# Optimization experiments

Measured on AMD Instinct MI355X. Metric: run time of the kernel, lower is better.

The kernel has to match this reference:

```python
import jax, jax.numpy as jnp
import numpy as np

N_NODES = 100000


def gcn_conv(x, edge_index, W, b, add_self_loops=True):
    """PyG GCNConv: out = D^{-1/2}(A+I)D^{-1/2} (x @ W) + b, sum-aggregated at col."""
    n = x.shape[0]
    x = x @ W  # linear first, like PyG (smaller feature dim usually)
    row, col = edge_index[0], edge_index[1]
    if add_self_loops:
        loop = jnp.arange(n, dtype=row.dtype)
        row = jnp.concatenate([row, loop])
        col = jnp.concatenate([col, loop])
    ones = jnp.ones(row.shape[0], dtype=x.dtype)
    deg = jax.ops.segment_sum(ones, col, num_segments=n)  # in-degree incl. self loops
    dinv = jnp.where(deg > 0, jax.lax.rsqrt(deg), 0.0)
    norm = dinv[row] * dinv[col]  # [E]
    msg = x[row] * norm[:, None]  # gather + scale, [E, F]
    out = jax.ops.segment_sum(msg, col, num_segments=n)  # scatter-add
    return out + b


def setup_inputs() -> dict:
    key = jax.random.key(0)
    ks = jax.random.split(key, 12)
    latent_dim, condition_dim, hidden_dim, output_dim = 64, 32, 64, 64
    n_edges = 1600000
    latent = jax.random.normal(ks[0], (N_NODES, latent_dim), dtype=jnp.float32)
    condition = jax.random.normal(ks[1], (N_NODES, condition_dim), dtype=jnp.float32)
    edge_index = jax.random.randint(ks[2], (2, n_edges), 0, N_NODES, dtype=jnp.int64 if jax.config.jax_enable_x64 else jnp.int32)

    def glorot(k, fan_in, fan_out):
        s = jnp.sqrt(6.0 / (fan_in + fan_out))
        return jax.random.uniform(k, (fan_in, fan_out), minval=-s, maxval=s, dtype=jnp.float32)

    W1 = glorot(ks[3], latent_dim, hidden_dim); b1 = jnp.zeros((hidden_dim,), jnp.float32)
    W2 = glorot(ks[4], condition_dim, hidden_dim); b2 = jnp.zeros((hidden_dim,), jnp.float32)
    W3 = glorot(ks[5], 2 * hidden_dim, hidden_dim); b3 = jnp.zeros((hidden_dim,), jnp.float32)
    W4 = glorot(ks[6], hidden_dim, output_dim); b4 = jnp.zeros((output_dim,), jnp.float32)
    return {"latent": latent, "condition": condition, "edge_index": edge_index,
            "W1": W1, "b1": b1, "W2": W2, "b2": b2,
            "W3": W3, "b3": b3, "W4": W4, "b4": b4}


def reference(latent, condition, edge_index, W1, b1, W2, b2, W3, b3, W4, b4):
    z2h = gcn_conv(latent, edge_index, W1, b1)
    c2h = gcn_conv(condition, edge_index, W2, b2)
    h = jnp.concatenate([z2h, c2h], axis=1)
    h = gcn_conv(h, edge_index, W3, b3)
    out = gcn_conv(h, edge_index, W4, b4)
    return out
```

## Files before the change

kernel.cpp:

```cpp
#include <hip/hip_runtime.h>
#include <hip/hip_fp16.h>

#define BKN 4
#define CBN 256
#define CHUNK 4096
#define MAXBIN 5120

typedef _Float16 half8 __attribute__((ext_vector_type(8)));
typedef _Float16 h4v __attribute__((ext_vector_type(4)));
typedef float floatx4 __attribute__((ext_vector_type(4)));


__global__ void init_cur_kernel(int* __restrict__ p, int n, int stride) {
    int i = blockIdx.x * blockDim.x + threadIdx.x;
    if (i < n) p[i] = i * stride;
}


__global__ __launch_bounds__(256) void passA_kernel(const int* __restrict__ ei,
                                                    int* __restrict__ curCB,
                                                    unsigned* __restrict__ binned,
                                                    int E, int NCB) {
    __shared__ int lcnt[512];
    __shared__ int sA[512], sB[512];
    __shared__ int loffx[512];
    __shared__ int gbase[512];
    __shared__ int lpos[512];
    __shared__ unsigned stage[CHUNK];
    __shared__ unsigned short sbin[CHUNK];
    int tid = threadIdx.x;
    int base = blockIdx.x * CHUNK;
    for (int i = tid; i < 512; i += 256) lcnt[i] = 0;
    __syncthreads();
    unsigned pk[16]; int bin[16];
    #pragma unroll
    for (int q = 0; q < 16; ++q) {
        int e = base + q * 256 + tid;
        if (e < E) {
            int r = ei[e], c = ei[E + e];
            pk[q] = ((unsigned)r << 8) | (unsigned)(c & 255);
            bin[q] = c >> 8;
            atomicAdd(&lcnt[bin[q]], 1);
        } else bin[q] = -1;
    }
    __syncthreads();
    for (int i = tid; i < 512; i += 256) sA[i] = lcnt[i];
    __syncthreads();
    int* src = sA; int* dst = sB;
    for (int o = 1; o < 512; o <<= 1) {
        for (int i = tid; i < 512; i += 256)
            dst[i] = src[i] + (i >= o ? src[i - o] : 0);
        __syncthreads();
        int* t = src; src = dst; dst = t;
    }
    for (int i = tid; i < 512; i += 256) {
        int ex = (i > 0) ? src[i - 1] : 0;
        loffx[i] = ex;
        lpos[i] = ex;
        int c = lcnt[i];
        gbase[i] = (c > 0 && i < NCB) ? atomicAdd(&curCB[i], c) : 0;
    }
    __syncthreads();
    #pragma unroll
    for (int q = 0; q < 16; ++q) {
        if (bin[q] >= 0) {
            int p = atomicAdd(&lpos[bin[q]], 1);
            stage[p] = pk[q];
            sbin[p] = (unsigned short)bin[q];
        }
    }
    __syncthreads();
    int total = min(CHUNK, E - base);
    for (int idx = tid; idx < total; idx += 256) {
        int b2 = sbin[idx];
        binned[gbase[b2] + (idx - loffx[b2])] = stage[idx];
    }
}


__global__ __launch_bounds__(256) void passB_kernel(const unsigned* __restrict__ binned,
                                                    const int* __restrict__ curCB,
                                                    int* __restrict__ bktR,
                                                    int* __restrict__ offN,
                                                    int* __restrict__ endN,
                                                    float* __restrict__ dinv,
                                                    int N, int NCB) {
    __shared__ unsigned raw[MAXBIN];
    __shared__ int stageR[MAXBIN];
    __shared__ int fcnt[256], foff[256], fpos[256];
    __shared__ int sA[256], sB[256];
    int i = blockIdx.x;
    int tid = threadIdx.x;
    int g0 = i * MAXBIN;
    int cnt = curCB[i] - g0;
    if (cnt > MAXBIN) cnt = MAXBIN;
    fcnt[tid] = 0;
    __syncthreads();
    for (int idx = tid; idx < cnt; idx += 256) {
        unsigned pk = binned[g0 + idx];
        raw[idx] = pk;
        atomicAdd(&fcnt[pk & 255], 1);
    }
    __syncthreads();
    sA[tid] = fcnt[tid];
    __syncthreads();
    int* src = sA; int* dst = sB;
    for (int o = 1; o < 256; o <<= 1) {
        dst[tid] = src[tid] + (tid >= o ? src[tid - o] : 0);
        __syncthreads();
        int* t = src; src = dst; dst = t;
    }
    int excl = src[tid] - fcnt[tid];
    foff[tid] = excl;
    fpos[tid] = excl;
    __syncthreads();
    for (int idx = tid; idx < cnt; idx += 256) {
        unsigned pk = raw[idx];
        int p = atomicAdd(&fpos[pk & 255], 1);
        stageR[p] = (int)(pk >> 8);
    }
    __syncthreads();
    for (int idx = tid; idx < cnt; idx += 256) bktR[g0 + idx] = stageR[idx];
    int n = i * CBN + tid;
    if (n < N) {
        offN[n] = g0 + foff[tid];
        endN[n] = g0 + foff[tid] + fcnt[tid];
        dinv[n] = rsqrtf((float)fcnt[tid] + 1.0f);
    }
}


__global__ __launch_bounds__(256) void fold_kernel(
    const float* __restrict__ W1, const float* __restrict__ b1,
    const float* __restrict__ W2, const float* __restrict__ b2,
    const float* __restrict__ W3, const float* __restrict__ b3,
    const float* __restrict__ W4,
    float* __restrict__ Wf1, float* __restrict__ Wf2,
    float* __restrict__ u, float* __restrict__ v) {
    __shared__ float As[64][64];
    __shared__ float gsl[64];
    int tid = threadIdx.x;
    int f = tid & 63;
    int w = __builtin_amdgcn_readfirstlane(tid >> 6);
    int blk = blockIdx.x;

    float w4c[64];
    #pragma unroll
    for (int k = 0; k < 64; ++k) w4c[k] = W4[k * 64 + f];

    if (blk < 24) {
        const int half = (blk < 16) ? 0 : 64;
        #pragma unroll 2
        for (int kk = 0; kk < 16; ++kk) {
            int k = w * 16 + kk;
            float a = 0.f;
            #pragma unroll
            for (int j = 0; j < 64; ++j)
                a += W3[(half + k) * 64 + j] * w4c[j];
            As[k][f] = a;
        }
        __syncthreads();
        const float* Wsrc = (blk < 16) ? W1 : W2;
        float* Wdst = (blk < 16) ? Wf1 : Wf2;
        int i = ((blk < 16) ? blk : (blk - 16)) * 4 + w;
        float a = 0.f;
        #pragma unroll
        for (int k = 0; k < 64; ++k)
            a += Wsrc[i * 64 + k] * As[k][f];
        Wdst[i * 64 + f] = a;
    } else {
        float g = 0.f;
        #pragma unroll
        for (int k = 0; k < 64; ++k) g += b1[k] * W3[k * 64 + f];
        #pragma unroll
        for (int k = 0; k < 64; ++k) g += b2[k] * W3[(64 + k) * 64 + f];
        if (w == 0) gsl[f] = g;
        __syncthreads();
        if (w == 0) {
            float uu = 0.f, vv = 0.f;
            #pragma unroll
            for (int k = 0; k < 64; ++k) {
                uu += gsl[k] * w4c[k];
                vv += b3[k] * w4c[k];
            }
            u[f] = uu;
            v[f] = vv;
        }
    }
}


__global__ __launch_bounds__(256) void linZ_kernel(
    const float* __restrict__ lat, const float* __restrict__ cond,
    const float* __restrict__ Wf1, const float* __restrict__ Wf2,
    const float* __restrict__ dinv, _Float16* __restrict__ Z, int N) {
    __shared__ _Float16 Xs[64][104];
    __shared__ _Float16 Wt[64][104];
    int tid = threadIdx.x;
    int n0 = blockIdx.x * 64;
    {
        const float4* lat4 = (const float4*)(lat + (size_t)n0 * 64);
        #pragma unroll
        for (int q = 0; q < 4; ++q) {
            int idx = q * 256 + tid;
            int row = idx >> 4;
            float4 v = make_float4(0.f, 0.f, 0.f, 0.f);
            if (n0 + row < N) v = lat4[idx];
            int col = (idx & 15) * 4;
            Xs[row][col + 0] = (_Float16)v.x;
            Xs[row][col + 1] = (_Float16)v.y;
            Xs[row][col + 2] = (_Float16)v.z;
            Xs[row][col + 3] = (_Float16)v.w;
        }
        const float4* cond4 = (const float4*)(cond + (size_t)n0 * 32);
        #pragma unroll
        for (int q = 0; q < 2; ++q) {
            int idx = q * 256 + tid;
            int row = idx >> 3;
            float4 v = make_float4(0.f, 0.f, 0.f, 0.f);
            if (n0 + row < N) v = cond4[idx];
            int col = 64 + (idx & 7) * 4;
            Xs[row][col + 0] = (_Float16)v.x;
            Xs[row][col + 1] = (_Float16)v.y;
            Xs[row][col + 2] = (_Float16)v.z;
            Xs[row][col + 3] = (_Float16)v.w;
        }
        for (int i = tid; i < 4096; i += 256) {
            int k = i >> 6, f = i & 63;
            Wt[f][k] = (_Float16)Wf1[i];
        }
        for (int i = tid; i < 2048; i += 256) {
            int k = i >> 6, f = i & 63;
            Wt[f][64 + k] = (_Float16)Wf2[i];
        }
    }
    __syncthreads();
    int lane = tid & 63, wave = tid >> 6;
    int quad = lane >> 4, l16 = lane & 15;
    floatx4 acc[4] = {};
    #pragma unroll
    for (int kc = 0; kc < 96; kc += 32) {
        half8 a = *(const half8*)&Xs[wave * 16 + l16][kc + quad * 8];
        #pragma unroll
        for (int nt = 0; nt < 4; ++nt) {
            half8 b = *(const half8*)&Wt[nt * 16 + l16][kc + quad * 8];
            acc[nt] = __builtin_amdgcn_mfma_f32_16x16x32_f16(a, b, acc[nt], 0, 0, 0);
        }
    }
    #pragma unroll
    for (int r = 0; r < 4; ++r) {
        int n = n0 + wave * 16 + quad * 4 + r;
        if (n < N) {
            float d = dinv[n];
            #pragma unroll
            for (int nt = 0; nt < 4; ++nt)
                Z[(size_t)n * 64 + nt * 16 + l16] = (_Float16)(acc[nt][r] * d);
        }
    }
}

template <bool FINAL>
__global__ __launch_bounds__(256) void hop_kernel(
    const _Float16* __restrict__ Vp, const float* __restrict__ dinv,
    const int* __restrict__ offN, const int* __restrict__ endN,
    const int* __restrict__ bktR,
    const float* __restrict__ wvec, void* __restrict__ outv, int NB) {
    int lane = threadIdx.x & 63;
    int wave = threadIdx.x >> 6;
    int b = blockIdx.x * 4 + wave;
    if (b >= NB) return;
    int g  = lane >> 4;
    int fq = lane & 15;
    int c0 = b * BKN;

    float res[4];
    #pragma unroll
    for (int t = 0; t < 4; ++t) {
        int n = c0 + t;
        int s = offN[n], e = endN[n];
        float a0, a1, a2, a3;
        {
            h4v h = *(const h4v*)&Vp[(size_t)n * 64 + fq * 4];
            float m = (g == 0) ? 1.f : 0.f;
            a0 = m * (float)h[0]; a1 = m * (float)h[1];
            a2 = m * (float)h[2]; a3 = m * (float)h[3];
        }
        #pragma unroll 2
        for (int i0 = s; i0 < e; i0 += 4) {
            int idx = i0 + g;
            int r = bktR[min(idx, e - 1)];
            h4v h = *(const h4v*)&Vp[(size_t)r * 64 + fq * 4];
            float m = (idx < e) ? 1.f : 0.f;
            a0 = fmaf(m, (float)h[0], a0);
            a1 = fmaf(m, (float)h[1], a1);
            a2 = fmaf(m, (float)h[2], a2);
            a3 = fmaf(m, (float)h[3], a3);
        }
        a0 += __shfl_xor(a0, 16, 64); a0 += __shfl_xor(a0, 32, 64);
        a1 += __shfl_xor(a1, 16, 64); a1 += __shfl_xor(a1, 32, 64);
        a2 += __shfl_xor(a2, 16, 64); a2 += __shfl_xor(a2, 32, 64);
        a3 += __shfl_xor(a3, 16, 64); a3 += __shfl_xor(a3, 32, 64);
        if (g == t) { res[0] = a0; res[1] = a1; res[2] = a2; res[3] = a3; }
    }

    int n = c0 + g;
    float d = dinv[n];
    float4 wv = *(const float4*)&wvec[fq * 4];
    if constexpr (FINAL) {
        float4 o;
        o.x = res[0] * d + wv.x;
        o.y = res[1] * d + wv.y;
        o.z = res[2] * d + wv.z;
        o.w = res[3] * d + wv.w;
        *(float4*)&((float*)outv)[(size_t)n * 64 + fq * 4] = o;
    } else {
        float dd = d * d;
        h4v o;
        o[0] = (_Float16)(res[0] * dd + d * wv.x);
        o[1] = (_Float16)(res[1] * dd + d * wv.y);
        o[2] = (_Float16)(res[2] * dd + d * wv.z);
        o[3] = (_Float16)(res[3] * dd + d * wv.w);
        *(h4v*)&((_Float16*)outv)[(size_t)n * 64 + fq * 4] = o;
    }
}


static inline size_t align256(size_t x) { return (x + 255) & ~(size_t)255; }

extern "C" void kernel_launch(void* const* d_in, const int* in_sizes, int n_in,
                              void* d_out, int out_size, void* d_ws, size_t ws_size,
                              hipStream_t stream) {
    const float* latent = (const float*)d_in[0];
    const float* cond   = (const float*)d_in[1];
    const int*   ei     = (const int*)d_in[2];
    const float* W1 = (const float*)d_in[3];
    const float* b1 = (const float*)d_in[4];
    const float* W2 = (const float*)d_in[5];
    const float* b2 = (const float*)d_in[6];
    const float* W3 = (const float*)d_in[7];
    const float* b3 = (const float*)d_in[8];
    const float* W4 = (const float*)d_in[9];
    const float* b4 = (const float*)d_in[10];
    float* out = (float*)d_out;

    const int N = in_sizes[0] / 64;
    const int E = in_sizes[2] / 2;
    const int NB  = (N + BKN - 1) / BKN;
    const int NCB = (N + CBN - 1) / CBN;
    const int NCH = (E + CHUNK - 1) / CHUNK;
    const size_t REG = (size_t)NCB * MAXBIN;

    char* w = (char*)d_ws;
    size_t o = 0;
    int* curCB = (int*)(w + o); o = align256(o + (size_t)NCB * 4);
    int* offN  = (int*)(w + o); o = align256(o + (size_t)N * 4);
    int* endN  = (int*)(w + o); o = align256(o + (size_t)N * 4);
    float* dinv = (float*)(w + o); o = align256(o + (size_t)N * 4);
    float* Wf1 = (float*)(w + o); o = align256(o + 4096 * 4);
    float* Wf2 = (float*)(w + o); o = align256(o + 2048 * 4);
    float* uVec = (float*)(w + o); o = align256(o + 64 * 4);
    float* vVec = (float*)(w + o); o = align256(o + 64 * 4);
    unsigned* binned = (unsigned*)(w + o); o = align256(o + REG * 4);
    int* bktR        = (int*)(w + o); o = align256(o + REG * 4);
    _Float16* Z = (_Float16*)(w + o); o = align256(o + (size_t)N * 64 * 2);
    _Float16* P = (_Float16*)(w + o); o = align256(o + (size_t)N * 64 * 2);

    const int BS = 256;
    int gHop = (NB + 3) / 4;

    init_cur_kernel<<<2, BS, 0, stream>>>(curCB, NCB, MAXBIN);
    passA_kernel<<<NCH, BS, 0, stream>>>(ei, curCB, binned, E, NCB);
    passB_kernel<<<NCB, BS, 0, stream>>>(binned, curCB, bktR, offN, endN, dinv, N, NCB);

    fold_kernel<<<25, BS, 0, stream>>>(W1, b1, W2, b2, W3, b3, W4, Wf1, Wf2, uVec, vVec);
    linZ_kernel<<<(N + 63) / 64, BS, 0, stream>>>(latent, cond, Wf1, Wf2, dinv, Z, N);

    hop_kernel<false><<<gHop, BS, 0, stream>>>(Z, dinv, offN, endN, bktR, uVec, (void*)P, NB);
    hop_kernel<false><<<gHop, BS, 0, stream>>>(P, dinv, offN, endN, bktR, vVec, (void*)Z, NB);
    hop_kernel<true ><<<gHop, BS, 0, stream>>>(Z, dinv, offN, endN, bktR, b4, (void*)out, NB);
}
```

Before: 286.0 us.

## Assign one node per 16-lane group in hop kernel with unrolled gathers

Changes the hop aggregation mapping: before, all 64 lanes worked on one node at a time, with the four 16-lane groups splitting that node's edges and then reducing across groups with shuffles. Now each 16-lane group owns one node and walks its whole edge list alone, using an 8-wide then 4-wide unrolled loop with several independent gathers in flight. This removes the masked tail iterations, the cross-group shuffle reductions and the serial loop over four nodes. In exchange, groups whose nodes have different degrees now diverge within a wave, and each group runs a longer serial loop over its own edges.

```diff
diff --git a/kernel.cpp b/kernel.cpp
--- a/kernel.cpp
+++ b/kernel.cpp
@@ -271,55 +271,71 @@
     if (b >= NB) return;
     int g  = lane >> 4;
     int fq = lane & 15;
-    int c0 = b * BKN;
-
-    float res[4];
-    #pragma unroll
-    for (int t = 0; t < 4; ++t) {
-        int n = c0 + t;
-        int s = offN[n], e = endN[n];
-        float a0, a1, a2, a3;
-        {
-            h4v h = *(const h4v*)&Vp[(size_t)n * 64 + fq * 4];
-            float m = (g == 0) ? 1.f : 0.f;
-            a0 = m * (float)h[0]; a1 = m * (float)h[1];
-            a2 = m * (float)h[2]; a3 = m * (float)h[3];
-        }
-        #pragma unroll 2
-        for (int i0 = s; i0 < e; i0 += 4) {
-            int idx = i0 + g;
-            int r = bktR[min(idx, e - 1)];
-            h4v h = *(const h4v*)&Vp[(size_t)r * 64 + fq * 4];
-            float m = (idx < e) ? 1.f : 0.f;
-            a0 = fmaf(m, (float)h[0], a0);
-            a1 = fmaf(m, (float)h[1], a1);
-            a2 = fmaf(m, (float)h[2], a2);
-            a3 = fmaf(m, (float)h[3], a3);
-        }
-        a0 += __shfl_xor(a0, 16, 64); a0 += __shfl_xor(a0, 32, 64);
-        a1 += __shfl_xor(a1, 16, 64); a1 += __shfl_xor(a1, 32, 64);
-        a2 += __shfl_xor(a2, 16, 64); a2 += __shfl_xor(a2, 32, 64);
-        a3 += __shfl_xor(a3, 16, 64); a3 += __shfl_xor(a3, 32, 64);
-        if (g == t) { res[0] = a0; res[1] = a1; res[2] = a2; res[3] = a3; }
-    }
-
-    int n = c0 + g;
+    int n = b * BKN + g;
+
+    float a0, a1, a2, a3;
+    {
+        h4v h = *(const h4v*)&Vp[(size_t)n * 64 + fq * 4];
+        a0 = (float)h[0]; a1 = (float)h[1]; a2 = (float)h[2]; a3 = (float)h[3];
+    }
+    int s = offN[n], e = endN[n];
+    int idx = s;
+    for (; idx + 8 <= e; idx += 8) {
+        int r0 = bktR[idx + 0], r1 = bktR[idx + 1];
+        int r2 = bktR[idx + 2], r3 = bktR[idx + 3];
+        int r4 = bktR[idx + 4], r5 = bktR[idx + 5];
+        int r6 = bktR[idx + 6], r7 = bktR[idx + 7];
+        h4v h0 = *(const h4v*)&Vp[(size_t)r0 * 64 + fq * 4];
+        h4v h1 = *(const h4v*)&Vp[(size_t)r1 * 64 + fq * 4];
+        h4v h2 = *(const h4v*)&Vp[(size_t)r2 * 64 + fq * 4];
+        h4v h3 = *(const h4v*)&Vp[(size_t)r3 * 64 + fq * 4];
+        h4v h4_ = *(const h4v*)&Vp[(size_t)r4 * 64 + fq * 4];
+        h4v h5 = *(const h4v*)&Vp[(size_t)r5 * 64 + fq * 4];
+        h4v h6 = *(const h4v*)&Vp[(size_t)r6 * 64 + fq * 4];
+        h4v h7 = *(const h4v*)&Vp[(size_t)r7 * 64 + fq * 4];
+        a0 += ((float)h0[0] + (float)h1[0]) + ((float)h2[0] + (float)h3[0])
+            + ((float)h4_[0] + (float)h5[0]) + ((float)h6[0] + (float)h7[0]);
+        a1 += ((float)h0[1] + (float)h1[1]) + ((float)h2[1] + (float)h3[1])
+            + ((float)h4_[1] + (float)h5[1]) + ((float)h6[1] + (float)h7[1]);
+        a2 += ((float)h0[2] + (float)h1[2]) + ((float)h2[2] + (float)h3[2])
+            + ((float)h4_[2] + (float)h5[2]) + ((float)h6[2] + (float)h7[2]);
+        a3 += ((float)h0[3] + (float)h1[3]) + ((float)h2[3] + (float)h3[3])
+            + ((float)h4_[3] + (float)h5[3]) + ((float)h6[3] + (float)h7[3]);
+    }
+    for (; idx + 4 <= e; idx += 4) {
+        int r0 = bktR[idx + 0], r1 = bktR[idx + 1];
+        int r2 = bktR[idx + 2], r3 = bktR[idx + 3];
+        h4v h0 = *(const h4v*)&Vp[(size_t)r0 * 64 + fq * 4];
+        h4v h1 = *(const h4v*)&Vp[(size_t)r1 * 64 + fq * 4];
+        h4v h2 = *(const h4v*)&Vp[(size_t)r2 * 64 + fq * 4];
+        h4v h3 = *(const h4v*)&Vp[(size_t)r3 * 64 + fq * 4];
+        a0 += ((float)h0[0] + (float)h1[0]) + ((float)h2[0] + (float)h3[0]);
+        a1 += ((float)h0[1] + (float)h1[1]) + ((float)h2[1] + (float)h3[1]);
+        a2 += ((float)h0[2] + (float)h1[2]) + ((float)h2[2] + (float)h3[2]);
+        a3 += ((float)h0[3] + (float)h1[3]) + ((float)h2[3] + (float)h3[3]);
+    }
+    for (; idx < e; ++idx) {
+        int r = bktR[idx];
+        h4v h = *(const h4v*)&Vp[(size_t)r * 64 + fq * 4];
+        a0 += (float)h[0]; a1 += (float)h[1]; a2 += (float)h[2]; a3 += (float)h[3];
+    }
+
     float d = dinv[n];
     float4 wv = *(const float4*)&wvec[fq * 4];
     if constexpr (FINAL) {
         float4 o;
-        o.x = res[0] * d + wv.x;
-        o.y = res[1] * d + wv.y;
-        o.z = res[2] * d + wv.z;
-        o.w = res[3] * d + wv.w;
+        o.x = a0 * d + wv.x;
+        o.y = a1 * d + wv.y;
+        o.z = a2 * d + wv.z;
+        o.w = a3 * d + wv.w;
         *(float4*)&((float*)outv)[(size_t)n * 64 + fq * 4] = o;
     } else {
         float dd = d * d;
         h4v o;
-        o[0] = (_Float16)(res[0] * dd + d * wv.x);
-        o[1] = (_Float16)(res[1] * dd + d * wv.y);
-        o[2] = (_Float16)(res[2] * dd + d * wv.z);
-        o[3] = (_Float16)(res[3] * dd + d * wv.w);
+        o[0] = (_Float16)(a0 * dd + d * wv.x);
+        o[1] = (_Float16)(a1 * dd + d * wv.y);
+        o[2] = (_Float16)(a2 * dd + d * wv.z);
+        o[3] = (_Float16)(a3 * dd + d * wv.w);
         *(h4v*)&((_Float16*)outv)[(size_t)n * 64 + fq * 4] = o;
     }
 }
```

New measurement: 260.2 us. -9.0%, faster.
